# Optimization experiments

Measured on AMD Instinct MI355X. Metric: run time of the kernel, lower is better.

## Reference

```python
import jax, jax.numpy as jnp
import numpy as np

B, T, D = 64, 48, 16          # batch, time_depth, input_dim (n variables)
H = 128                       # n_units (== N_units, forced by decomp: y=h_mix has width n_units)
NU = 128                      # N_units
HEADS = 8
HEAD_DIM = H // HEADS
THR = 0.01                    # attention_threshold
LAM = 0.01                    # ridge_lambda
SHORT = 2

# All off-diagonal variable pairs. The torch code gathers only pairs in the batch-union of
# (a_t > 0) & ~eye; using ALL off-diagonal pairs is mathematically identical because excluded
# pairs have a_t == 0 for every batch element, giving all-zero phi columns whose ridge
# coefficients are exactly 0 and which do not perturb the other coefficients or h_hat.
_I, _J = np.nonzero(~np.eye(D, dtype=bool))
I_IDX = jnp.asarray(_I)
J_IDX = jnp.asarray(_J)
P = D * (D - 1)
K = 2 * D + P


def setup_inputs() -> dict:
    key = jax.random.key(0)
    ks = jax.random.split(key, 32)
    f32 = jnp.float32
    n = lambda k, shp, s: (jax.random.normal(k, shp, f32) * s)
    inp = {
        'x': jax.random.normal(ks[0], (B, T, D), f32),
        # per-variable LSTM params
        'W_j': n(ks[1], (D, H, H), 1.0 / np.sqrt(H)),
        'W_i': n(ks[2], (D, H, H), 1.0 / np.sqrt(H)),
        'W_f': n(ks[3], (D, H, H), 1.0 / np.sqrt(H)),
        'W_o': n(ks[4], (D, H, H), 1.0 / np.sqrt(H)),
        'U_j': n(ks[5], (D, 1, H), 0.3),
        'U_i': n(ks[6], (D, 1, H), 0.3),
        'U_f': n(ks[7], (D, 1, H), 0.3),
        'U_o': n(ks[8], (D, 1, H), 0.3),
        'B_j': jnp.full((D, H), 0.01, f32),
        'B_i': jnp.full((D, H), 0.01, f32),
        'B_f': jnp.full((D, H), 0.01, f32),
        'B_o': jnp.full((D, H), 0.01, f32),
        # mix LSTM params
        'u_j': n(ks[9], (D, NU), 0.3),
        'u_i': n(ks[10], (D, NU), 0.3),
        'u_f': n(ks[11], (D, NU), 0.3),
        'u_o': n(ks[12], (D, NU), 0.3),
        'w_j': n(ks[13], (NU, NU), 1.0 / np.sqrt(NU)),
        'w_i': n(ks[14], (NU, NU), 1.0 / np.sqrt(NU)),
        'w_f': n(ks[15], (NU, NU), 1.0 / np.sqrt(NU)),
        'w_o': n(ks[16], (NU, NU), 1.0 / np.sqrt(NU)),
        'b_j': jnp.full((NU,), 0.01, f32),
        'b_i': jnp.full((NU,), 0.01, f32),
        'b_f': jnp.full((NU,), 0.01, f32),
        'b_o': jnp.full((NU,), 0.01, f32),
        # attention params (torch Linear convention: y = x @ W.T)
        'W_qkv': n(ks[17], (3 * H, H), 1.0 / np.sqrt(H)),
        'W_out': n(ks[18], (H, H), 1.0 / np.sqrt(H)),
        # interaction decomposition psi projection
        'W_psi': n(ks[19], (H, H), 1.0 / np.sqrt(H)),
        'b_psi': jnp.full((H,), 0.01, f32),
        # prediction head
        'w_p': n(ks[20], (H, 1), 1.0 / np.sqrt(H)),
        'b_p': jnp.full((1,), 0.01, f32),
    }
    return inp


def _forward(x, W_j, W_i, W_f, W_o, U_j, U_i, U_f, U_o, B_j, B_i, B_f, B_o,
             u_j, u_i, u_f, u_o, w_j, w_i, w_f, w_o, b_j, b_i, b_f, b_o,
             W_qkv, W_out, W_psi, b_psi, w_p, b_p):
    f32 = x.dtype
    eyeK = LAM * jnp.eye(K, dtype=f32)

    def var_gate(h_var, x_t, W, U, Bp):
        # torch einsum('bij,ijk->bik') + einsum('bij,jik->bjk') with x_t unsqueezed
        return jnp.einsum('bdh,dhk->bdk', h_var, W) + x_t[:, :, None] * U[:, 0, :] + Bp

    def step(carry, inp):
        h_var, c_var, h_mix, c_mix = carry
        x_t, t = inp  # x_t: [B, D]
        h_prev = h_var
        # per-variable tensorized LSTM
        j_var = jnp.tanh(var_gate(h_var, x_t, W_j, U_j, B_j))
        i_var = jax.nn.sigmoid(var_gate(h_var, x_t, W_i, U_i, B_i))
        f_var = jax.nn.sigmoid(var_gate(h_var, x_t, W_f, U_f, B_f))
        o_var = jax.nn.sigmoid(var_gate(h_var, x_t, W_o, U_o, B_o))
        c_var = c_var * f_var + i_var * j_var
        h_var = o_var * jnp.tanh(c_var)
        delta_h = h_var - h_prev
        # mix LSTM
        i_t = jax.nn.sigmoid(x_t @ u_i + h_mix @ w_i + b_i)
        f_t = jax.nn.sigmoid(x_t @ u_f + h_mix @ w_f + b_f)
        o_t = jax.nn.sigmoid(x_t @ u_o + h_mix @ w_o + b_o)
        j_t = jnp.tanh(x_t @ u_j + h_mix @ w_j + b_j)
        c_mix = f_t * c_mix + i_t * j_t
        h_mix_lstm = o_t * jnp.tanh(c_mix)
        # multi-head cross-variable attention over the D variables
        qkv = h_var @ W_qkv.T                                  # [B, D, 3H]
        q, k, v = jnp.split(qkv, 3, axis=-1)
        q = q.reshape(B, D, HEADS, HEAD_DIM).transpose(0, 2, 1, 3)
        k = k.reshape(B, D, HEADS, HEAD_DIM).transpose(0, 2, 1, 3)
        v = v.reshape(B, D, HEADS, HEAD_DIM).transpose(0, 2, 1, 3)
        scores = jnp.einsum('bhqe,bhke->bhqk', q, k) / np.sqrt(HEAD_DIM).astype(np.float32)
        attn = jax.nn.softmax(scores, axis=-1)
        attn = jnp.where(attn >= THR, attn, jnp.zeros_like(attn))  # hard threshold, no renorm
        ctx = jnp.einsum('bhqk,bhke->bhqe', attn, v)
        ctx = ctx.transpose(0, 2, 1, 3).reshape(B, D, H)
        z = ctx @ W_out.T                                      # [B, D, H]
        a_t = attn.mean(axis=1)                                # [B, D, D]
        phi_long = jnp.swapaxes(h_prev, 1, 2)                  # [B, H, D]
        phi_short = jnp.swapaxes(delta_h, 1, 2)                # [B, H, D]
        pair = z[:, I_IDX, :] * z[:, J_IDX, :]                 # [B, P, H]
        psi = jnp.tanh(pair @ W_psi.T + b_psi)                 # [B, P, H]
        w = a_t[:, I_IDX, J_IDX][..., None]                    # [B, P, 1]
        phi_inter = jnp.swapaxes(psi * w, 1, 2)                # [B, H, P]
        phi = jnp.concatenate([phi_long, phi_short, phi_inter], axis=2)  # [B, H, K]
        A = jnp.einsum('bhk,bhl->bkl', phi, phi) + eyeK        # [B, K, K]
        bvec = jnp.einsum('bhk,bh->bk', phi, h_mix_lstm)       # [B, K]
        theta = jnp.linalg.solve(A, bvec[..., None])[..., 0]   # [B, K]
        h_hat = jnp.einsum('bhk,bk->bh', phi, theta)           # [B, H]
        alpha = theta[:, :D]
        beta = theta[:, D:2 * D]
        gamma = jnp.zeros((B, D, D), f32).at[:, I_IDX, J_IDX].set(theta[:, 2 * D:])
        pred_y = h_hat @ w_p + b_p                             # [B, 1]
        h_mix_new = jnp.where(t > SHORT, h_hat, h_mix_lstm)
        return (h_var, c_var, h_mix_new, c_mix), (pred_y, alpha, beta, gamma)

    h_var0 = jnp.zeros((B, D, H), f32)
    c_var0 = jnp.zeros((B, D, H), f32)
    h_mix0 = jnp.zeros((B, NU), f32)
    c_mix0 = jnp.zeros((B, NU), f32)
    ts = jnp.arange(T - 1)
    xs = (jnp.swapaxes(x, 0, 1)[:T - 1], ts)
    _, (preds, alphas, betas, gammas) = jax.lax.scan(step, (h_var0, c_var0, h_mix0, c_mix0), xs)
    s = SHORT + 1
    pred = jnp.swapaxes(preds[s:], 0, 1)   # [B, T-SHORT-2, 1]
    return pred, alphas[s:], betas[s:], gammas[s:]


def reference(x, W_j, W_i, W_f, W_o, U_j, U_i, U_f, U_o, B_j, B_i, B_f, B_o,
              u_j, u_i, u_f, u_o, w_j, w_i, w_f, w_o, b_j, b_i, b_f, b_o,
              W_qkv, W_out, W_psi, b_psi, w_p, b_p):
    return _forward(x, W_j, W_i, W_f, W_o, U_j, U_i, U_f, U_o, B_j, B_i, B_f, B_o,
                    u_j, u_i, u_f, u_o, w_j, w_i, w_f, w_o, b_j, b_i, b_f, b_o,
                    W_qkv, W_out, W_psi, b_psi, w_p, b_p)
```

## Files before the change

### kernel.cpp

```cpp
#include <hip/hip_runtime.h>
#include <hip/hip_bf16.h>
#include <math.h>

#define B_ 64
#define T_ 48
#define D_ 16
#define H_ 128
#define NU_ 128
#define LAM_ 0.01f
#define THR_ 0.01f

#define NSTEP_OUT 44
#define OFF_A (B_*NSTEP_OUT)
#define OFF_B (OFF_A + NSTEP_OUT*B_*D_)
#define OFF_G (OFF_B + NSTEP_OUT*B_*D_)

#define PHI_ROWS 240
#define PHI_STR  (PHI_ROWS*H_)
#define PHIBUF   (B_*PHI_STR)
#define GW_STR   12288
#define GBUF     (B_*GW_STR)
#define L_STR    16896
#define LBUF     (B_*L_STR)
#define PLS_STR  4096
#define PLSBUF   (B_*PLS_STR)

#define QKS 388
#define SCS 264

__device__ __forceinline__ float sigm(float v) { return 1.0f / (1.0f + expf(-v)); }
__device__ __forceinline__ float dot4(float4 a, float4 b) {
    return a.x*b.x + a.y*b.y + a.z*b.z + a.w*b.w;
}
__device__ __forceinline__ float rdlane(float v, int l) {
    return __uint_as_float(__builtin_amdgcn_readlane(__float_as_uint(v), l));
}


__global__ __launch_bounds__(256) void k_P(
    float* __restrict__ hv, float* __restrict__ cv,
    const float* __restrict__ gates, float* __restrict__ pls,
    const float* __restrict__ Wqkv, const float* __restrict__ Wout,
    float* __restrict__ z, float* __restrict__ at_g,
    const float* __restrict__ phi, float* __restrict__ Gring,
    const float* __restrict__ Lring,
    const float* __restrict__ hml, float* __restrict__ h_mix,
    const float* __restrict__ w_p, const float* __restrict__ b_p,
    float* __restrict__ out, int t)
{
    __shared__ __align__(16) float smem[12416];
    const int tid = threadIdx.x;
    const int bx = blockIdx.x;

    if (bx < 64) {
        const int ta = t + 2;
        if (ta < 0 || ta > T_ - 2) return;
        const int b = bx;
        const int BDH = B_*D_*H_;
        float* hs = smem;
        float* qk = smem + 2048;
        float* sc = smem + 8256;
        float* cx = smem + 10368;

        float* plsb = pls + ((size_t)(ta&3))*PLSBUF + (size_t)b*PLS_STR;
        const float4* g0 = (const float4*)(gates + b*2048);
        const float4* g1 = (const float4*)(gates + BDH + b*2048);
        const float4* g2 = (const float4*)(gates + 2*BDH + b*2048);
        const float4* g3 = (const float4*)(gates + 3*BDH + b*2048);
        float4* cv4 = (float4*)(cv + b*2048);
        float4* hv4 = (float4*)(hv + b*2048);
        float4* pl0 = (float4*)plsb;
        float4* pl1 = (float4*)(plsb + 16*H_);
        #pragma unroll
        for (int i = 0; i < 2; ++i) {
            int e4 = i*256 + tid;
            float4 jv = g0[e4], iv = g1[e4], fv = g2[e4], ov = g3[e4];
            float4 c = cv4[e4], ho = hv4[e4];
            float4 cn, hn, dl;
            cn.x = c.x*fv.x + iv.x*jv.x; hn.x = ov.x*tanhf(cn.x); dl.x = hn.x - ho.x;
            cn.y = c.y*fv.y + iv.y*jv.y; hn.y = ov.y*tanhf(cn.y); dl.y = hn.y - ho.y;
            cn.z = c.z*fv.z + iv.z*jv.z; hn.z = ov.z*tanhf(cn.z); dl.z = hn.z - ho.z;
            cn.w = c.w*fv.w + iv.w*jv.w; hn.w = ov.w*tanhf(cn.w); dl.w = hn.w - ho.w;
            cv4[e4] = cn; hv4[e4] = hn;
            ((float4*)hs)[e4] = hn;
            pl0[e4] = ho;
            pl1[e4] = dl;
        }
        __syncthreads();

        {
            const int half = tid >> 7, mt = tid & 127;
            const float4* w0 = (const float4*)(Wqkv + (size_t)(mt*3 + 0)*H_);
            const float4* w1 = (const float4*)(Wqkv + (size_t)(mt*3 + 1)*H_);
            const float4* w2 = (const float4*)(Wqkv + (size_t)(mt*3 + 2)*H_);
            float acc[3][8] = {};
            for (int i4 = 0; i4 < 32; i4++) {
                float4 wa = w0[i4], wb = w1[i4], wc = w2[i4];
                #pragma unroll
                for (int rr = 0; rr < 8; rr++) {
                    float4 h4 = *(const float4*)&hs[(half*8 + rr)*128 + i4*4];
                    acc[0][rr] += dot4(wa, h4);
                    acc[1][rr] += dot4(wb, h4);
                    acc[2][rr] += dot4(wc, h4);
                }
            }
            #pragma unroll
            for (int q = 0; q < 3; q++)
                #pragma unroll
                for (int rr = 0; rr < 8; rr++)
                    qk[(half*8 + rr)*QKS + mt*3 + q] = acc[q][rr];
        }
        __syncthreads();

        for (int e = tid; e < 2048; e += 256) {
            int hh2 = e >> 8, qd = (e >> 4) & 15, kd = e & 15;
            float s = 0.f;
            #pragma unroll
            for (int e4 = 0; e4 < 4; e4++)
                s += dot4(*(const float4*)&qk[qd*QKS + hh2*16 + e4*4],
                          *(const float4*)&qk[kd*QKS + 128 + hh2*16 + e4*4]);
            sc[hh2*SCS + qd*16 + kd] = s * 0.25f;
        }
        __syncthreads();

        if (tid < 128) {
            int hh2 = tid >> 4, qd = tid & 15;
            float mx = -1e30f;
            #pragma unroll
            for (int kd = 0; kd < 16; kd++) mx = fmaxf(mx, sc[hh2*SCS + qd*16 + kd]);
            float ex[16]; float s = 0.f;
            #pragma unroll
            for (int kd = 0; kd < 16; kd++) { ex[kd] = expf(sc[hh2*SCS + qd*16 + kd] - mx); s += ex[kd]; }
            float inv = 1.0f / s;
            #pragma unroll
            for (int kd = 0; kd < 16; kd++) {
                float a = ex[kd]*inv;
                sc[hh2*SCS + qd*16 + kd] = (a >= THR_) ? a : 0.0f;
            }
        }
        __syncthreads();

        {
            int qd = tid >> 4, kd = tid & 15;
            float s = 0.f;
            #pragma unroll
            for (int hh2 = 0; hh2 < 8; hh2++) s += sc[hh2*SCS + qd*16 + kd];
            at_g[b*256 + qd*16 + kd] = s * 0.125f;
        }

        for (int e = tid; e < 2048; e += 256) {
            int qd = e >> 7, c = e & 127, hh2 = c >> 4, ee = c & 15;
            float s = 0.f;
            #pragma unroll
            for (int kd = 0; kd < 16; kd++) s += sc[hh2*SCS + qd*16 + kd] * qk[kd*QKS + 256 + hh2*16 + ee];
            cx[qd*128 + c] = s;
        }
        __syncthreads();

        {
            int h = tid & 127, half = tid >> 7;
            const float4* wr = (const float4*)(Wout + (size_t)h*H_);
            float acc[8] = {};
            for (int i4 = 0; i4 < 32; i4++) {
                float4 w4 = wr[i4];
                #pragma unroll
                for (int r = 0; r < 8; r++)
                    acc[r] += dot4(w4, *(const float4*)&cx[(half*8 + r)*128 + i4*4]);
            }
            #pragma unroll
            for (int r = 0; r < 8; r++) z[b*2048 + (half*8 + r)*H_ + h] = acc[r];
        }
    } else if (bx < 256) {
        const int tg = t + 1;
        if (tg < 3 || tg > T_ - 2) return;
        const int tile = (bx - 64) >> 6, b = (bx - 64) & 63;
        const int r0 = (tile >= 1) ? 64 : 0;
        const int c0 = (tile == 2) ? 64 : 0;
        const bool diag = (r0 == c0);
        float* prt = smem;
        float* pct = smem + 1024;
        const float* pb   = phi + ((size_t)(tg%3))*PHIBUF + (size_t)b*PHI_STR;
        const float* plsb = pls + ((size_t)(tg&3))*PLSBUF + (size_t)b*PLS_STR;
        const int tr = tid >> 4, tc = tid & 15;
        const int kk = tid >> 4, rr4 = (tid & 15) << 2;
        float acc[4][4] = {};
        float4 vr, vc;

        {
            const float* src = (kk < 32) ? (plsb + (size_t)kk*H_) : (pb + (size_t)(kk - 32)*H_);
            vr = *(const float4*)&src[r0 + rr4];
            if (!diag) vc = *(const float4*)&src[c0 + rr4];
        }
        for (int kt = 0; kt < 17; kt++) {
            *(float4*)&prt[kk*64 + rr4] = vr;
            if (!diag) *(float4*)&pct[kk*64 + rr4] = vc;
            __syncthreads();
            if (kt < 16) {
                int krow = (kt + 1)*16 + kk;
                const float* src = (krow < 32) ? (plsb + (size_t)krow*H_)
                                               : (pb + (size_t)(krow - 32)*H_);
                vr = *(const float4*)&src[r0 + rr4];
                if (!diag) vc = *(const float4*)&src[c0 + rr4];
            }
            const float* pcb = diag ? prt : pct;
            #pragma unroll
            for (int k2 = 0; k2 < 16; k2++) {
                float4 a4 = *(const float4*)&prt[k2*64 + tr*4];
                float4 b4 = *(const float4*)&pcb[k2*64 + tc*4];
                float av[4] = {a4.x, a4.y, a4.z, a4.w};
                float bv[4] = {b4.x, b4.y, b4.z, b4.w};
                #pragma unroll
                for (int i = 0; i < 4; i++)
                    #pragma unroll
                    for (int j = 0; j < 4; j++)
                        acc[i][j] += av[i]*bv[j];
            }
            __syncthreads();
        }
        float* Gt = Gring + ((size_t)(tg&1))*GBUF + (size_t)b*GW_STR + (size_t)tile*4096;
        #pragma unroll
        for (int i = 0; i < 4; i++) {
            int lr = tr*4 + i;
            float v[4];
            #pragma unroll
            for (int j = 0; j < 4; j++) {
                int lc = tc*4 + j;
                v[j] = acc[i][j] + ((diag && lr == lc) ? LAM_ : 0.0f);
            }
            float4 o; o.x = v[0]; o.y = v[1]; o.z = v[2]; o.w = v[3];
            *(float4*)&Gt[lr*64 + tc*4] = o;
        }
    } else {
        const int tv = t - 1;
        if (tv < 0 || tv > T_ - 2) return;
        const int b = bx - 256;
        if (tv < 3) {
            if (tid < 128) h_mix[b*128 + tid] = hml[b*128 + tid];
            return;
        }
        float* ys = smem;
        const float* Lb = Lring + ((size_t)(tv&1))*LBUF + (size_t)b*L_STR;

        if (tid < 64) {
            __builtin_amdgcn_s_setprio(1);
            const int lane = tid;
            float hm0 = hml[b*128 + lane];
            float hm1 = hml[b*128 + lane + 64];
            float dv0 = Lb[lane*132 + 128];
            float dv1 = Lb[(lane+64)*132 + 128];
            float acc0 = hm0, acc1 = hm1;

            {
                float c0[16], c1[16], n0[16], n1[16];
                #pragma unroll
                for (int k = 0; k < 16; ++k) {
                    c0[k] = Lb[k*132 + lane];
                    c1[k] = Lb[k*132 + lane + 64];
                }
                for (int g = 0; g < 4; ++g) {
                    if (g < 3) {
                        #pragma unroll
                        for (int k = 0; k < 16; ++k) {
                            n0[k] = Lb[(16*(g+1)+k)*132 + lane];
                            n1[k] = Lb[(16*(g+1)+k)*132 + lane + 64];
                        }
                    }
                    const int s = 16*g;
                    #pragma unroll
                    for (int k = 0; k < 16; ++k) {
                        int j = s + k;
                        float yj = rdlane(acc0 * dv0, j);
                        if (lane > j) acc0 -= c0[k]*yj;
                        else if (lane == j) acc0 = yj;
                        acc1 -= c1[k]*yj;
                    }
                    #pragma unroll
                    for (int k = 0; k < 16; ++k) { c0[k] = n0[k]; c1[k] = n1[k]; }
                }
            }
            {
                float c1[16], n1[16];
                #pragma unroll
                for (int k = 0; k < 16; ++k) c1[k] = Lb[(64+k)*132 + lane + 64];
                for (int g = 0; g < 4; ++g) {
                    if (g < 3) {
                        #pragma unroll
                        for (int k = 0; k < 16; ++k)
                            n1[k] = Lb[(64+16*(g+1)+k)*132 + lane + 64];
                    }
                    #pragma unroll
                    for (int k = 0; k < 16; ++k) {
                        int j = 16*g + k;
                        float yj = rdlane(acc1 * dv1, j);
                        if (lane > j) acc1 -= c1[k]*yj;
                        else if (lane == j) acc1 = yj;
                    }
                    #pragma unroll
                    for (int k = 0; k < 16; ++k) c1[k] = n1[k];
                }
            }
            ys[lane] = acc0;
            ys[lane + 64] = acc1;

            for (int p = 7; p >= 0; --p) {
                const int s = p*16;
                float br = 0.f, minv = 0.f;
                float lc[16];
                if (lane < 16) {
                    br = ys[s + lane];
                    minv = Lb[(s+lane)*132 + 128];
                    #pragma unroll
                    for (int k4 = 0; k4 < 4; ++k4) {
                        float4 f4 = *(const float4*)&Lb[(s+lane)*132 + s + k4*4];
                        lc[k4*4+0]=f4.x; lc[k4*4+1]=f4.y; lc[k4*4+2]=f4.z; lc[k4*4+3]=f4.w;
                    }
                } else {
                    #pragma unroll
                    for (int k = 0; k < 16; ++k) lc[k] = 0.f;
                }
                float xk[16];
                #pragma unroll
                for (int j = 15; j >= 0; --j) {
                    if (lane == j) br *= minv;
                    float xj = rdlane(br, j);
                    if (lane < j) br -= lc[j]*xj;
                    xk[j] = xj;
                }
                if (lane < 16) ys[s + lane] = br;
                for (int i = lane; i < s; i += 64) {
                    float a = ys[i];
                    #pragma unroll
                    for (int k4 = 0; k4 < 4; ++k4) {
                        float4 f4 = *(const float4*)&Lb[i*132 + s + k4*4];
                        a -= f4.x*xk[k4*4] + f4.y*xk[k4*4+1] + f4.z*xk[k4*4+2] + f4.w*xk[k4*4+3];
                    }
                    ys[i] = a;
                }
            }

            float y0 = ys[lane], y1 = ys[lane + 64];
            float hh0 = hm0 - LAM_*y0, hh1 = hm1 - LAM_*y1;
            h_mix[b*128 + lane]      = hh0;
            h_mix[b*128 + lane + 64] = hh1;
            float pw = hh0 * w_p[lane] + hh1 * w_p[lane + 64];
            for (int off = 32; off; off >>= 1) pw += __shfl_down(pw, off);
            if (lane == 0) out[b*NSTEP_OUT + (tv - 3)] = pw + b_p[0];
            __builtin_amdgcn_s_setprio(0);
        }
        __syncthreads();

        {
            const int ts = tv - 3;
            const float* plsb = pls + ((size_t)(tv&3))*PLSBUF + (size_t)b*PLS_STR;
            const float* phb  = phi + ((size_t)(tv%3))*PHIBUF + (size_t)b*PHI_STR;
            const float4* y4  = (const float4*)ys;
            for (int k = tid; k < 272; k += 256) {
                const float* rowp = (k < 32) ? plsb + (size_t)k*H_
                                             : phb + (size_t)(k - 32)*H_;
                const float4* r4 = (const float4*)rowp;
                float th = 0.f;
                #pragma unroll
                for (int i4 = 0; i4 < 32; i4++) th += dot4(r4[i4], y4[i4]);
                if (k < 16)
                    out[OFF_A + ts*(B_*D_) + b*D_ + k] = th;
                else if (k < 32)
                    out[OFF_B + ts*(B_*D_) + b*D_ + (k - 16)] = th;
                else {
                    int p = k - 32, ip = p/15, jj = p%15, jp = jj + (jj >= ip ? 1 : 0);
                    out[OFF_G + ts*(B_*D_*D_) + b*(D_*D_) + ip*D_ + jp] = th;
                }
            }
            if (tid < D_)
                out[OFF_G + ts*(B_*D_*D_) + b*(D_*D_) + tid*D_ + tid] = 0.0f;
        }
    }
}

__global__ __launch_bounds__(256) void k_Q(
    const float* __restrict__ z, const float* __restrict__ at,
    const float* __restrict__ Wpsi, const float* __restrict__ bpsi,
    float* __restrict__ phi,
    const float* __restrict__ x, const float* __restrict__ hv,
    const float* __restrict__ Wj, const float* __restrict__ Wi, const float* __restrict__ Wf, const float* __restrict__ Wo,
    const float* __restrict__ Uj, const float* __restrict__ Ui, const float* __restrict__ Uf, const float* __restrict__ Uo,
    const float* __restrict__ Bj, const float* __restrict__ Bi, const float* __restrict__ Bf, const float* __restrict__ Bo,
    float* __restrict__ gates,
    const float* __restrict__ Gring, float* __restrict__ Lring,
    const float* __restrict__ h_mix, float* __restrict__ c_mix, float* __restrict__ hml,
    const float* __restrict__ uj, const float* __restrict__ ui, const float* __restrict__ uf, const float* __restrict__ uo,
    const float* __restrict__ wj, const float* __restrict__ wi, const float* __restrict__ wf, const float* __restrict__ wo,
    const float* __restrict__ bj, const float* __restrict__ bi, const float* __restrict__ bf_, const float* __restrict__ bo,
    int t)
{
    __shared__ __align__(16) float smem[8448];
    const int tid = threadIdx.x;
    const int bx = blockIdx.x;

    if (bx < 128) {
        const int tf = t + (bx >> 6);
        if ((t & 1) || tf < 3 || tf > T_ - 2) return;
        const int b = bx & 63;
        float* Pan = smem;

        const int R = tid >> 4, C = tid & 15;
        const bool lower = (C <= R);

        float g[8][8] = {};
        if (lower) {
            const int tsel = (C >= 8) ? 2 : ((R >= 8) ? 1 : 0);
            const float* Gt = Gring + ((size_t)(tf&1))*GBUF + (size_t)b*GW_STR + (size_t)tsel*4096;
            const int lcb = C*8 - ((C >= 8) ? 64 : 0);
            #pragma unroll
            for (int r = 0; r < 8; ++r) {
                const int lr = R*8 + r - ((R >= 8) ? 64 : 0);
                float4 lo = *(const float4*)(Gt + lr*64 + lcb);
                float4 hi = *(const float4*)(Gt + lr*64 + lcb + 4);
                g[r][0]=lo.x; g[r][1]=lo.y; g[r][2]=lo.z; g[r][3]=lo.w;
                g[r][4]=hi.x; g[r][5]=hi.y; g[r][6]=hi.z; g[r][7]=hi.w;
            }
        }

        float* Lb = Lring + ((size_t)(tf&1))*LBUF + (size_t)b*L_STR;

        for (int p = 0; p < 8; ++p) {
            const int s = p*16;
            if ((C >> 1) == p && R >= 2*p) {
                #pragma unroll
                for (int c = 0; c < 8; ++c) {
                    const int lc = ((C & 1) << 3) + c;
                    float4 lo = {g[0][c], g[1][c], g[2][c], g[3][c]};
                    float4 hi = {g[4][c], g[5][c], g[6][c], g[7][c]};
                    *(float4*)&Pan[lc*132 + R*8]     = lo;
                    *(float4*)&Pan[lc*132 + R*8 + 4] = hi;
                }
            }
            __syncthreads();
            if (tid < 64) {
                const int lane = tid;
                const int r0 = s + lane, r1 = r0 + 64;
                const bool v0 = r0 < 128, v1 = r1 < 128;
                float a0[16], a1[16];
                #pragma unroll
                for (int k = 0; k < 16; ++k) {
                    a0[k] = v0 ? Pan[k*132 + r0] : 0.f;
                    a1[k] = v1 ? Pan[k*132 + r1] : 0.f;
                }
                float myinv = 0.f;
                #pragma unroll
                for (int j = 0; j < 16; ++j) {
                    float piv = rdlane(a0[j], j);
                    float inv = rsqrtf(piv);
                    float dsq = piv * inv;
                    if (lane == j) myinv = inv;
                    a0[j] = (lane == j) ? dsq : a0[j]*inv;
                    a1[j] *= inv;
                    #pragma unroll
                    for (int c = j+1; c < 16; ++c) {
                        float Lcj = rdlane(a0[j], c);
                        a0[c] -= a0[j]*Lcj;
                        a1[c] -= a1[j]*Lcj;
                    }
                }
                if (lane < 16) Lb[(s+lane)*132 + 128] = myinv;
                #pragma unroll
                for (int k = 0; k < 16; ++k) {
                    if (v0) { Pan[k*132 + r0] = a0[k]; Lb[(s+k)*132 + r0] = a0[k]; }
                    if (v1) { Pan[k*132 + r1] = a1[k]; Lb[(s+k)*132 + r1] = a1[k]; }
                }
            }
            __syncthreads();
            if (lower && C >= 2*(p+1)) {
                const float* colp = Pan;
                float4 r04 = *(const float4*)&colp[R*8];
                float4 r14 = *(const float4*)&colp[R*8 + 4];
                float4 c04 = *(const float4*)&colp[C*8];
                float4 c14 = *(const float4*)&colp[C*8 + 4];
                #pragma unroll
                for (int k = 0; k < 16; ++k) {
                    float lr[8] = {r04.x,r04.y,r04.z,r04.w,r14.x,r14.y,r14.z,r14.w};
                    float lc[8] = {c04.x,c04.y,c04.z,c04.w,c14.x,c14.y,c14.z,c14.w};
                    if (k < 15) {
                        const float* coln = &Pan[(k+1)*132];
                        r04 = *(const float4*)&coln[R*8];
                        r14 = *(const float4*)&coln[R*8 + 4];
                        c04 = *(const float4*)&coln[C*8];
                        c14 = *(const float4*)&coln[C*8 + 4];
                    }
                    #pragma unroll
                    for (int r = 0; r < 8; ++r)
                        #pragma unroll
                        for (int c = 0; c < 8; ++c)
                            g[r][c] -= lr[r]*lc[c];
                }
            }
            __syncthreads();
        }
    } else if (bx < 448) {
        const int tp = t + 2;
        if (tp < 3 || tp > T_ - 2) return;
        const int pc = (bx - 128) >> 6, b = (bx - 128) & 63;
        const int p0 = pc * 48;
        float* zs = smem;
        float* pr = smem + 2048;

        {
            const float4* zsrc = (const float4*)(z + b*2048);
            #pragma unroll
            for (int i = 0; i < 2; ++i) ((float4*)zs)[i*256 + tid] = zsrc[i*256 + tid];
        }
        __syncthreads();
        for (int e = tid; e < 48*128; e += 256) {
            int pp = e >> 7, c = e & 127;
            int p = p0 + pp, ip = p/15, jj2 = p%15, jp = jj2 + (jj2 >= ip ? 1 : 0);
            pr[pp*128 + c] = zs[ip*128 + c] * zs[jp*128 + c];
        }
        __syncthreads();

        const int hg = tid & 31, pg = tid >> 5;
        const int h0 = hg*4, pp0 = pg*6;
        const float4* w0 = (const float4*)(Wpsi + (size_t)(h0+0)*H_);
        const float4* w1 = (const float4*)(Wpsi + (size_t)(h0+1)*H_);
        const float4* w2 = (const float4*)(Wpsi + (size_t)(h0+2)*H_);
        const float4* w3 = (const float4*)(Wpsi + (size_t)(h0+3)*H_);
        float acc[6][4] = {};
        for (int i4 = 0; i4 < 32; i4++) {
            float4 wa = w0[i4], wb = w1[i4], wc = w2[i4], wd = w3[i4];
            #pragma unroll
            for (int r = 0; r < 6; r++) {
                float4 p4 = *(const float4*)&pr[(pp0 + r)*128 + i4*4];
                acc[r][0] += dot4(wa, p4);
                acc[r][1] += dot4(wb, p4);
                acc[r][2] += dot4(wc, p4);
                acc[r][3] += dot4(wd, p4);
            }
        }
        float4 bb = *(const float4*)&bpsi[h0];
        float* phb = phi + ((size_t)(tp%3))*PHIBUF + (size_t)b*PHI_STR;
        #pragma unroll
        for (int r = 0; r < 6; r++) {
            int pp = pp0 + r, p = p0 + pp;
            int ip = p/15, jj2 = p%15, jp = jj2 + (jj2 >= ip ? 1 : 0);
            float wat = at[b*256 + ip*16 + jp];
            float4 o;
            o.x = tanhf(acc[r][0] + bb.x) * wat;
            o.y = tanhf(acc[r][1] + bb.y) * wat;
            o.z = tanhf(acc[r][2] + bb.z) * wat;
            o.w = tanhf(acc[r][3] + bb.w) * wat;
            *(float4*)&phb[(size_t)p*H_ + h0] = o;
        }
    } else if (bx < 576) {
        const int tn = t + 3;
        if (tn < 0 || tn > T_ - 2) return;
        float* hsT = smem;
        float* Ws  = smem + 4352;
        const int fbx = bx - 448;
        const int kh = fbx & 1, g = (fbx >> 1) & 3, d = fbx >> 3;
        const int k0 = kh * 64;
        const float* W  = (g==0?Wj:(g==1?Wi:(g==2?Wf:Wo))) + (size_t)d*H_*H_;
        const float* U  = (g==0?Uj:(g==1?Ui:(g==2?Uf:Uo))) + d*H_;
        const float* Bp = (g==0?Bj:(g==1?Bi:(g==2?Bf:Bo))) + d*H_;

        const int tb = tid >> 4, tk = tid & 15;
        float acc[4][4] = {};

        for (int hc = 0; hc < 2; hc++) {
            __syncthreads();
            for (int e = tid; e < 64*64; e += 256) {
                int b2 = e >> 6, h2 = e & 63;
                hsT[h2*68 + b2] = hv[(b2*D_ + d)*H_ + hc*64 + h2];
            }
            for (int e = tid; e < 64*64; e += 256) {
                int h2 = e >> 6, kk = e & 63;
                Ws[h2*64 + kk] = W[(hc*64 + h2)*H_ + k0 + kk];
            }
            __syncthreads();
            for (int h2 = 0; h2 < 64; h2++) {
                float4 hb = *(const float4*)&hsT[h2*68 + tb*4];
                float4 wk = *(const float4*)&Ws[h2*64 + tk*4];
                float hbv[4] = {hb.x, hb.y, hb.z, hb.w};
                float wkv[4] = {wk.x, wk.y, wk.z, wk.w};
                #pragma unroll
                for (int a2 = 0; a2 < 4; a2++)
                    #pragma unroll
                    for (int c2 = 0; c2 < 4; c2++)
                        acc[a2][c2] += hbv[a2] * wkv[c2];
            }
        }

        float u4[4], bp4[4];
        #pragma unroll
        for (int c2 = 0; c2 < 4; c2++) { u4[c2] = U[k0 + tk*4 + c2]; bp4[c2] = Bp[k0 + tk*4 + c2]; }

        #pragma unroll
        for (int a2 = 0; a2 < 4; a2++) {
            int b2 = tb*4 + a2;
            float xv = x[(b2*T_ + tn)*D_ + d];
            float4 o;
            float pre[4];
            #pragma unroll
            for (int c2 = 0; c2 < 4; c2++) pre[c2] = acc[a2][c2] + xv*u4[c2] + bp4[c2];
            if (g == 0) { o.x = tanhf(pre[0]); o.y = tanhf(pre[1]); o.z = tanhf(pre[2]); o.w = tanhf(pre[3]); }
            else        { o.x = sigm(pre[0]);  o.y = sigm(pre[1]);  o.z = sigm(pre[2]);  o.w = sigm(pre[3]); }
            *(float4*)&gates[(size_t)g*(B_*D_*H_) + (b2*D_ + d)*H_ + k0 + tk*4] = o;
        }
    } else {
        const int tm = t;
        if (tm < 0 || tm > T_ - 2) return;
        const int b = bx - 576;
        float* xs  = smem;
        float* hs2 = smem + 16;
        float* gj  = smem + 144;
        float* gi  = smem + 272;
        float* gf  = smem + 400;
        float* go  = smem + 528;
        const int n = tid & 127, gg = tid >> 7;
        if (tid < 16)  xs[tid]  = x[(b*T_ + tm)*D_ + tid];
        if (tid < 128) hs2[tid] = h_mix[b*NU_ + tid];
        __syncthreads();

        const float* uA = gg ? uf : uj;
        const float* uB = gg ? uo : ui;
        const float* wA = gg ? wf : wj;
        const float* wB = gg ? wo : wi;
        float accA = gg ? bf_[n] : bj[n];
        float accB = gg ? bo[n]  : bi[n];
        #pragma unroll
        for (int d2 = 0; d2 < 16; ++d2) {
            float xv = xs[d2];
            accA += xv * uA[d2*NU_ + n];
            accB += xv * uB[d2*NU_ + n];
        }
        for (int m = 0; m < 128; ++m) {
            float hvv = hs2[m];
            accA += hvv * wA[m*NU_ + n];
            accB += hvv * wB[m*NU_ + n];
        }
        if (gg == 0) { gj[n] = tanhf(accA); gi[n] = sigm(accB); }
        else         { gf[n] = sigm(accA);  go[n] = sigm(accB); }
        __syncthreads();
        if (tid < 128) {
            float cn = gf[tid]*c_mix[b*NU_ + tid] + gi[tid]*gj[tid];
            c_mix[b*NU_ + tid] = cn;
            hml[b*NU_ + tid]   = go[tid]*tanhf(cn);
        }
    }
}


__global__ __launch_bounds__(256) void k_X8(
    float* __restrict__ hv, float* __restrict__ cv,
    const float* __restrict__ gates, float* __restrict__ pls,
    const float* __restrict__ Wqkv, const float* __restrict__ Wout,
    float* __restrict__ z, float* __restrict__ at_g,
    const float* __restrict__ phi, float* __restrict__ Gw,
    const float* __restrict__ x, const float* __restrict__ h_mix,
    float* __restrict__ c_mix, float* __restrict__ hml,
    const float* __restrict__ uj, const float* __restrict__ ui, const float* __restrict__ uf, const float* __restrict__ uo,
    const float* __restrict__ wj, const float* __restrict__ wi, const float* __restrict__ wf, const float* __restrict__ wo,
    const float* __restrict__ bj, const float* __restrict__ bi, const float* __restrict__ bf_, const float* __restrict__ bo,
    const float* __restrict__ ybuf, float* __restrict__ out,
    int ta, int tg, int tm, int te)
{
    __shared__ __align__(16) float smem[12416];
    const int tid = threadIdx.x;
    const int bx = blockIdx.x;

    if (bx < 64) {
        if (ta < 0) return;
        const int b = bx;
        const int BDH = B_*D_*H_;
        float* hs = smem;
        float* qk = smem + 2048;
        float* sc = smem + 8256;
        float* cx = smem + 10368;

        float* plsb = pls + ((size_t)(ta&3)*B_ + b)*PLS_STR;
        const float4* g0 = (const float4*)(gates + b*2048);
        const float4* g1 = (const float4*)(gates + BDH + b*2048);
        const float4* g2 = (const float4*)(gates + 2*BDH + b*2048);
        const float4* g3 = (const float4*)(gates + 3*BDH + b*2048);
        float4* cv4 = (float4*)(cv + b*2048);
        float4* hv4 = (float4*)(hv + b*2048);
        float4* pl0 = (float4*)plsb;
        float4* pl1 = (float4*)(plsb + 16*H_);
        #pragma unroll
        for (int i = 0; i < 2; ++i) {
            int e4 = i*256 + tid;
            float4 jv = g0[e4], iv = g1[e4], fv = g2[e4], ov = g3[e4];
            float4 c = cv4[e4], ho = hv4[e4];
            float4 cn, hn, dl;
            cn.x = c.x*fv.x + iv.x*jv.x; hn.x = ov.x*tanhf(cn.x); dl.x = hn.x - ho.x;
            cn.y = c.y*fv.y + iv.y*jv.y; hn.y = ov.y*tanhf(cn.y); dl.y = hn.y - ho.y;
            cn.z = c.z*fv.z + iv.z*jv.z; hn.z = ov.z*tanhf(cn.z); dl.z = hn.z - ho.z;
            cn.w = c.w*fv.w + iv.w*jv.w; hn.w = ov.w*tanhf(cn.w); dl.w = hn.w - ho.w;
            cv4[e4] = cn; hv4[e4] = hn;
            ((float4*)hs)[e4] = hn;
            pl0[e4] = ho;
            pl1[e4] = dl;
        }
        __syncthreads();
        {
            const int half = tid >> 7, mt = tid & 127;
            const float4* w0 = (const float4*)(Wqkv + (size_t)(mt*3 + 0)*H_);
            const float4* w1 = (const float4*)(Wqkv + (size_t)(mt*3 + 1)*H_);
            const float4* w2 = (const float4*)(Wqkv + (size_t)(mt*3 + 2)*H_);
            float acc[3][8] = {};
            for (int i4 = 0; i4 < 32; i4++) {
                float4 wa = w0[i4], wb = w1[i4], wc = w2[i4];
                #pragma unroll
                for (int rr = 0; rr < 8; rr++) {
                    float4 h4 = *(const float4*)&hs[(half*8 + rr)*128 + i4*4];
                    acc[0][rr] += dot4(wa, h4);
                    acc[1][rr] += dot4(wb, h4);
                    acc[2][rr] += dot4(wc, h4);
                }
            }
            #pragma unroll
            for (int q = 0; q < 3; q++)
                #pragma unroll
                for (int rr = 0; rr < 8; rr++)
                    qk[(half*8 + rr)*QKS + mt*3 + q] = acc[q][rr];
        }
        __syncthreads();
        for (int e = tid; e < 2048; e += 256) {
            int hh2 = e >> 8, qd = (e >> 4) & 15, kd = e & 15;
            float s = 0.f;
            #pragma unroll
            for (int e4 = 0; e4 < 4; e4++)
                s += dot4(*(const float4*)&qk[qd*QKS + hh2*16 + e4*4],
                          *(const float4*)&qk[kd*QKS + 128 + hh2*16 + e4*4]);
            sc[hh2*SCS + qd*16 + kd] = s * 0.25f;
        }
        __syncthreads();
        if (tid < 128) {
            int hh2 = tid >> 4, qd = tid & 15;
            float mx = -1e30f;
            #pragma unroll
            for (int kd = 0; kd < 16; kd++) mx = fmaxf(mx, sc[hh2*SCS + qd*16 + kd]);
            float ex[16]; float s = 0.f;
            #pragma unroll
            for (int kd = 0; kd < 16; kd++) { ex[kd] = expf(sc[hh2*SCS + qd*16 + kd] - mx); s += ex[kd]; }
            float inv = 1.0f / s;
            #pragma unroll
            for (int kd = 0; kd < 16; kd++) {
                float a = ex[kd]*inv;
                sc[hh2*SCS + qd*16 + kd] = (a >= THR_) ? a : 0.0f;
            }
        }
        __syncthreads();
        {
            int qd = tid >> 4, kd = tid & 15;
            float s = 0.f;
            #pragma unroll
            for (int hh2 = 0; hh2 < 8; hh2++) s += sc[hh2*SCS + qd*16 + kd];
            at_g[b*256 + qd*16 + kd] = s * 0.125f;
        }
        for (int e = tid; e < 2048; e += 256) {
            int qd = e >> 7, c = e & 127, hh2 = c >> 4, ee = c & 15;
            float s = 0.f;
            #pragma unroll
            for (int kd = 0; kd < 16; kd++) s += sc[hh2*SCS + qd*16 + kd] * qk[kd*QKS + 256 + hh2*16 + ee];
// ... 330 lines not shown
            const float4* zsrc = (const float4*)(z + b*2048);
            #pragma unroll
            for (int i = 0; i < 2; ++i) ((float4*)zs)[i*256 + tid] = zsrc[i*256 + tid];
        }
        __syncthreads();
        for (int e = tid; e < 48*128; e += 256) {
            int pp = e >> 7, c = e & 127;
            int p = p0 + pp, ip = p/15, jj2 = p%15, jp = jj2 + (jj2 >= ip ? 1 : 0);
            pr[pp*128 + c] = zs[ip*128 + c] * zs[jp*128 + c];
        }
        __syncthreads();
        const int hg = tid & 31, pg = tid >> 5;
        const int h0 = hg*4, pp0 = pg*6;
        const float4* w0 = (const float4*)(Wpsi + (size_t)(h0+0)*H_);
        const float4* w1 = (const float4*)(Wpsi + (size_t)(h0+1)*H_);
        const float4* w2 = (const float4*)(Wpsi + (size_t)(h0+2)*H_);
        const float4* w3 = (const float4*)(Wpsi + (size_t)(h0+3)*H_);
        float acc[6][4] = {};
        for (int i4 = 0; i4 < 32; i4++) {
            float4 wa = w0[i4], wb = w1[i4], wc = w2[i4], wd = w3[i4];
            #pragma unroll
            for (int r = 0; r < 6; r++) {
                float4 p4 = *(const float4*)&pr[(pp0 + r)*128 + i4*4];
                acc[r][0] += dot4(wa, p4);
                acc[r][1] += dot4(wb, p4);
                acc[r][2] += dot4(wc, p4);
                acc[r][3] += dot4(wd, p4);
            }
        }
        float4 bb = *(const float4*)&bpsi[h0];
        float* phb = phi + (size_t)(tp&1)*PHIBUF + (size_t)b*PHI_STR;
        #pragma unroll
        for (int r = 0; r < 6; r++) {
            int pp = pp0 + r, p = p0 + pp;
            int ip = p/15, jj2 = p%15, jp = jj2 + (jj2 >= ip ? 1 : 0);
            float wat = at[b*256 + ip*16 + jp];
            float4 o;
            o.x = tanhf(acc[r][0] + bb.x) * wat;
            o.y = tanhf(acc[r][1] + bb.y) * wat;
            o.z = tanhf(acc[r][2] + bb.z) * wat;
            o.w = tanhf(acc[r][3] + bb.w) * wat;
            *(float4*)&phb[(size_t)p*H_ + h0] = o;
        }
    } else {
        if (tf < 0 || tf > T_ - 2) return;
        float* hsT = smem;
        float* Ws  = smem + 8704;
        const int fbx = bx - 384;
        const int kh = fbx & 1, g = (fbx >> 1) & 3, d = fbx >> 3;
        const int k0 = kh * 64;
        const float* W  = (g==0?Wj:(g==1?Wi:(g==2?Wf:Wo))) + (size_t)d*H_*H_;
        const float* U  = (g==0?Uj:(g==1?Ui:(g==2?Uf:Uo))) + d*H_;
        const float* Bp = (g==0?Bj:(g==1?Bi:(g==2?Bf:Bo))) + d*H_;

        for (int e = tid; e < 64*128; e += 256) {
            int b2 = e >> 7, h2 = e & 127;
            hsT[h2*68 + b2] = hv[(b2*D_ + d)*H_ + h2];
        }
        const int tb = tid >> 4, tk = tid & 15;
        float acc[4][4] = {};
        for (int hc = 0; hc < 2; hc++) {
            __syncthreads();
            for (int e = tid; e < 64*64; e += 256) {
                int h2 = e >> 6, kk = e & 63;
                Ws[h2*64 + kk] = W[(hc*64 + h2)*H_ + k0 + kk];
            }
            __syncthreads();
            for (int h2 = 0; h2 < 64; h2++) {
                float4 hb = *(const float4*)&hsT[(hc*64 + h2)*68 + tb*4];
                float4 wk = *(const float4*)&Ws[h2*64 + tk*4];
                float hbv[4] = {hb.x, hb.y, hb.z, hb.w};
                float wkv[4] = {wk.x, wk.y, wk.z, wk.w};
                #pragma unroll
                for (int a2 = 0; a2 < 4; a2++)
                    #pragma unroll
                    for (int c2 = 0; c2 < 4; c2++)
                        acc[a2][c2] += hbv[a2] * wkv[c2];
            }
        }
        float u4[4], bp4[4];
        #pragma unroll
        for (int c2 = 0; c2 < 4; c2++) { u4[c2] = U[k0 + tk*4 + c2]; bp4[c2] = Bp[k0 + tk*4 + c2]; }
        #pragma unroll
        for (int a2 = 0; a2 < 4; a2++) {
            int b2 = tb*4 + a2;
            float xv = x[(b2*T_ + tf)*D_ + d];
            float4 o;
            float pre[4];
            #pragma unroll
            for (int c2 = 0; c2 < 4; c2++) pre[c2] = acc[a2][c2] + xv*u4[c2] + bp4[c2];
            if (g == 0) { o.x = tanhf(pre[0]); o.y = tanhf(pre[1]); o.z = tanhf(pre[2]); o.w = tanhf(pre[3]); }
            else        { o.x = sigm(pre[0]);  o.y = sigm(pre[1]);  o.z = sigm(pre[2]);  o.w = sigm(pre[3]); }
            *(float4*)&gates[(size_t)g*(B_*D_*H_) + (b2*D_ + d)*H_ + k0 + tk*4] = o;
        }
    }
}

extern "C" void kernel_launch(void* const* d_in, const int* in_sizes, int n_in,
                              void* d_out, int out_size, void* d_ws, size_t ws_size,
                              hipStream_t stream) {
    const float* x    = (const float*)d_in[0];
    const float* W_j  = (const float*)d_in[1];
    const float* W_i  = (const float*)d_in[2];
    const float* W_f  = (const float*)d_in[3];
    const float* W_o  = (const float*)d_in[4];
    const float* U_j  = (const float*)d_in[5];
    const float* U_i  = (const float*)d_in[6];
    const float* U_f  = (const float*)d_in[7];
    const float* U_o  = (const float*)d_in[8];
    const float* B_j  = (const float*)d_in[9];
    const float* B_i  = (const float*)d_in[10];
    const float* B_f  = (const float*)d_in[11];
    const float* B_o  = (const float*)d_in[12];
    const float* u_j  = (const float*)d_in[13];
    const float* u_i  = (const float*)d_in[14];
    const float* u_f  = (const float*)d_in[15];
    const float* u_o  = (const float*)d_in[16];
    const float* w_j  = (const float*)d_in[17];
    const float* w_i  = (const float*)d_in[18];
    const float* w_f  = (const float*)d_in[19];
    const float* w_o  = (const float*)d_in[20];
    const float* b_j  = (const float*)d_in[21];
    const float* b_i  = (const float*)d_in[22];
    const float* b_f  = (const float*)d_in[23];
    const float* b_o  = (const float*)d_in[24];
    const float* W_qkv= (const float*)d_in[25];
    const float* W_out= (const float*)d_in[26];
    const float* W_psi= (const float*)d_in[27];
    const float* b_psi= (const float*)d_in[28];
    const float* w_p  = (const float*)d_in[29];
    const float* b_p  = (const float*)d_in[30];

    float* out = (float*)d_out;
    float* ws = (float*)d_ws;

    const size_t NEED = (size_t)11640832 * 4;

    if (ws_size >= NEED) {
        float* hv    = ws;
        float* cv    = hv + 131072;
        float* h_mix = cv + 131072;
        float* c_mix = h_mix + 8192;
        float* hml   = c_mix + 8192;
        float* gates = hml + 8192;
        float* zbuf  = gates + 524288;
        float* atbuf = zbuf + 131072;
        float* pls   = atbuf + 16384;
        float* phi   = pls + 4*262144;
        float* Gring = phi + (size_t)3*1966080;
        float* Lring = Gring + 2*786432;

        hipMemsetAsync(ws, 0, (size_t)286720 * sizeof(float), stream);

        #define LAUNCH_P(tt) k_P<<<320, 256, 0, stream>>>( \
            hv, cv, gates, pls, W_qkv, W_out, zbuf, atbuf, phi, Gring, Lring, \
            hml, h_mix, w_p, b_p, out, (tt))
        #define LAUNCH_Q(tt) k_Q<<<640, 256, 0, stream>>>( \
            zbuf, atbuf, W_psi, b_psi, phi, x, hv, \
            W_j, W_i, W_f, W_o, U_j, U_i, U_f, U_o, B_j, B_i, B_f, B_o, gates, \
            Gring, Lring, h_mix, c_mix, hml, \
            u_j, u_i, u_f, u_o, w_j, w_i, w_f, w_o, b_j, b_i, b_f, b_o, (tt))

        LAUNCH_Q(-3);
        LAUNCH_P(-2);
        LAUNCH_Q(-2);
        LAUNCH_P(-1);
        LAUNCH_Q(-1);

        for (int t = 0; t <= 47; ++t) {
            LAUNCH_P(t);
            if (t < 47) LAUNCH_Q(t);
        }
        #undef LAUNCH_P
        #undef LAUNCH_Q
    } else {
        float* h_var = ws;
        float* c_var = h_var + 131072;
        float* h_mix = c_var + 131072;
        float* c_mix = h_mix + 8192;
        float* hml   = c_mix + 8192;
        float* gates = hml + 8192;
        float* phi   = gates + 524288;
        float* zbuf  = phi + 3932160;
        float* atbuf = zbuf + 131072;
        float* Gw    = atbuf + 16384;
        float* pls   = Gw + 786432;
        float* ybuf  = pls + 1048576;

        hipMemsetAsync(ws, 0, (size_t)278528 * sizeof(float), stream);

        k_Y8<<<512, 256, 0, stream>>>(
            zbuf, atbuf, W_psi, b_psi, phi, x, h_var,
            W_j, W_i, W_f, W_o, U_j, U_i, U_f, U_o, B_j, B_i, B_f, B_o, gates,
            Gw, hml, h_mix, w_p, b_p, ybuf, out, -1, 0, -1);

        for (int t = 0; t < T_ - 1; t++) {
            k_X8<<<448, 256, 0, stream>>>(
                h_var, c_var, gates, pls, W_qkv, W_out, zbuf, atbuf,
                phi, Gw, x, h_mix, c_mix, hml,
                u_j, u_i, u_f, u_o, w_j, w_i, w_f, w_o, b_j, b_i, b_f, b_o,
                ybuf, out, t, t - 1, t - 1, t - 2);
            k_Y8<<<512, 256, 0, stream>>>(
                zbuf, atbuf, W_psi, b_psi, phi, x, h_var,
                W_j, W_i, W_f, W_o, U_j, U_i, U_f, U_o, B_j, B_i, B_f, B_o, gates,
                Gw, hml, h_mix, w_p, b_p, ybuf, out, t, t + 1, t - 1);
        }
        k_X8<<<448, 256, 0, stream>>>(
            h_var, c_var, gates, pls, W_qkv, W_out, zbuf, atbuf,
            phi, Gw, x, h_mix, c_mix, hml,
            u_j, u_i, u_f, u_o, w_j, w_i, w_f, w_o, b_j, b_i, b_f, b_o,
            ybuf, out, -1, T_ - 2, T_ - 2, T_ - 3);
        k_Y8<<<512, 256, 0, stream>>>(
            zbuf, atbuf, W_psi, b_psi, phi, x, h_var,
            W_j, W_i, W_f, W_o, U_j, U_i, U_f, U_o, B_j, B_i, B_f, B_o, gates,
            Gw, hml, h_mix, w_p, b_p, ybuf, out, -1, -1, T_ - 2);
        k_X8<<<448, 256, 0, stream>>>(
            h_var, c_var, gates, pls, W_qkv, W_out, zbuf, atbuf,
            phi, Gw, x, h_mix, c_mix, hml,
            u_j, u_i, u_f, u_o, w_j, w_i, w_f, w_o, b_j, b_i, b_f, b_o,
            ybuf, out, -1, -1, -1, T_ - 2);
    }
}
```

Baseline: 3.367 ms.

## Move blocked Cholesky factorization from k_Q into k_P, one timestep per launch

The per-batch blocked Cholesky of the ridge Gram matrix moves out of k_Q, where it ran on alternate steps for two timesteps at once, into extra blocks of k_P that factor one timestep per launch. The shared-memory panel is double-buffered, which drops the trailing barrier per panel. Each factored panel is copied to the global L buffer with a coalesced float4 copy instead of scattered per-lane stores. The aim is to even out per-step critical-path work and cut barrier and store overhead, at the cost of a longer-running k_P and a dependence on G being ready one launch earlier.

```diff
diff --git a/kernel.cpp b/kernel.cpp
--- a/kernel.cpp
+++ b/kernel.cpp
@@ -43,7 +43,7 @@
     const float* __restrict__ Wqkv, const float* __restrict__ Wout,
     float* __restrict__ z, float* __restrict__ at_g,
     const float* __restrict__ phi, float* __restrict__ Gring,
-    const float* __restrict__ Lring,
+    float* __restrict__ Lring,
     const float* __restrict__ hml, float* __restrict__ h_mix,
     const float* __restrict__ w_p, const float* __restrict__ b_p,
     float* __restrict__ out, int t)
@@ -230,7 +230,7 @@
             float4 o; o.x = v[0]; o.y = v[1]; o.z = v[2]; o.w = v[3];
             *(float4*)&Gt[lr*64 + tc*4] = o;
         }
-    } else {
+    } else if (bx < 320) {
         const int tv = t - 1;
         if (tv < 0 || tv > T_ - 2) return;
         const int b = bx - 256;
@@ -373,6 +373,110 @@
             if (tid < D_)
                 out[OFF_G + ts*(B_*D_*D_) + b*(D_*D_) + tid*D_ + tid] = 0.0f;
         }
+    } else {
+        const int tf = t;
+        if (tf < 3 || tf > T_ - 2) return;
+        const int b = bx - 320;
+        float* Pan = smem;
+
+        const int R = tid >> 4, C = tid & 15;
+        const bool lower = (C <= R);
+
+        float g[8][8] = {};
+        if (lower) {
+            const int tsel = (C >= 8) ? 2 : ((R >= 8) ? 1 : 0);
+            const float* Gt = Gring + ((size_t)(tf&1))*GBUF + (size_t)b*GW_STR + (size_t)tsel*4096;
+            const int lcb = C*8 - ((C >= 8) ? 64 : 0);
+            #pragma unroll
+            for (int r = 0; r < 8; ++r) {
+                const int lr = R*8 + r - ((R >= 8) ? 64 : 0);
+                float4 lo = *(const float4*)(Gt + lr*64 + lcb);
+                float4 hi = *(const float4*)(Gt + lr*64 + lcb + 4);
+                g[r][0]=lo.x; g[r][1]=lo.y; g[r][2]=lo.z; g[r][3]=lo.w;
+                g[r][4]=hi.x; g[r][5]=hi.y; g[r][6]=hi.z; g[r][7]=hi.w;
+            }
+        }
+
+        float* Lb = Lring + ((size_t)(tf&1))*LBUF + (size_t)b*L_STR;
+
+        for (int p = 0; p < 8; ++p) {
+            const int s = p*16;
+            float* Pc = Pan + (p & 1)*2112;
+            if ((C >> 1) == p && R >= 2*p) {
+                #pragma unroll
+                for (int c = 0; c < 8; ++c) {
+                    const int lc = ((C & 1) << 3) + c;
+                    float4 lo = {g[0][c], g[1][c], g[2][c], g[3][c]};
+                    float4 hi = {g[4][c], g[5][c], g[6][c], g[7][c]};
+                    *(float4*)&Pc[lc*132 + R*8]     = lo;
+                    *(float4*)&Pc[lc*132 + R*8 + 4] = hi;
+                }
+            }
+            __syncthreads();
+            if (tid < 64) {
+                const int lane = tid;
+                const int r0 = s + lane, r1 = r0 + 64;
+                const bool v0 = r0 < 128, v1 = r1 < 128;
+                float a0[16], a1[16];
+                #pragma unroll
+                for (int k = 0; k < 16; ++k) {
+                    a0[k] = v0 ? Pc[k*132 + r0] : 0.f;
+                    a1[k] = v1 ? Pc[k*132 + r1] : 0.f;
+                }
+                float myinv = 0.f;
+                #pragma unroll
+                for (int j = 0; j < 16; ++j) {
+                    float piv = rdlane(a0[j], j);
+                    float inv = rsqrtf(piv);
+                    float dsq = piv * inv;
+                    if (lane == j) myinv = inv;
+                    a0[j] = (lane == j) ? dsq : a0[j]*inv;
+                    a1[j] *= inv;
+                    #pragma unroll
+                    for (int c = j+1; c < 16; ++c) {
+                        float Lcj = rdlane(a0[j], c);
+                        a0[c] -= a0[j]*Lcj;
+                        a1[c] -= a1[j]*Lcj;
+                    }
+                }
+                if (lane < 16) Pc[lane*132 + 128] = myinv;
+                #pragma unroll
+                for (int k = 0; k < 16; ++k) {
+                    if (v0) Pc[k*132 + r0] = a0[k];
+                    if (v1) Pc[k*132 + r1] = a1[k];
+                }
+            }
+            __syncthreads();
+            {
+                const float4* s4 = (const float4*)Pc;
+                float4* d4 = (float4*)(Lb + (size_t)s*132);
+                for (int e = tid; e < 528; e += 256) d4[e] = s4[e];
+            }
+            if (lower && C >= 2*(p+1)) {
+                const float* colp = Pc;
+                float4 r04 = *(const float4*)&colp[R*8];
+                float4 r14 = *(const float4*)&colp[R*8 + 4];
+                float4 c04 = *(const float4*)&colp[C*8];
+                float4 c14 = *(const float4*)&colp[C*8 + 4];
+                #pragma unroll
+                for (int k = 0; k < 16; ++k) {
+                    float lr[8] = {r04.x,r04.y,r04.z,r04.w,r14.x,r14.y,r14.z,r14.w};
+                    float lc[8] = {c04.x,c04.y,c04.z,c04.w,c14.x,c14.y,c14.z,c14.w};
+                    if (k < 15) {
+                        const float* coln = &Pc[(k+1)*132];
+                        r04 = *(const float4*)&coln[R*8];
+                        r14 = *(const float4*)&coln[R*8 + 4];
+                        c04 = *(const float4*)&coln[C*8];
+                        c14 = *(const float4*)&coln[C*8 + 4];
+                    }
+                    #pragma unroll
+                    for (int r = 0; r < 8; ++r)
+                        #pragma unroll
+                        for (int c = 0; c < 8; ++c)
+                            g[r][c] -= lr[r]*lc[c];
+                }
+            }
+        }
     }
 }
 
@@ -385,7 +489,6 @@
     const float* __restrict__ Uj, const float* __restrict__ Ui, const float* __restrict__ Uf, const float* __restrict__ Uo,
     const float* __restrict__ Bj, const float* __restrict__ Bi, const float* __restrict__ Bf, const float* __restrict__ Bo,
     float* __restrict__ gates,
-    const float* __restrict__ Gring, float* __restrict__ Lring,
     const float* __restrict__ h_mix, float* __restrict__ c_mix, float* __restrict__ hml,
     const float* __restrict__ uj, const float* __restrict__ ui, const float* __restrict__ uf, const float* __restrict__ uo,
     const float* __restrict__ wj, const float* __restrict__ wi, const float* __restrict__ wf, const float* __restrict__ wo,
@@ -396,109 +499,10 @@
     const int tid = threadIdx.x;
     const int bx = blockIdx.x;
 
-    if (bx < 128) {
-        const int tf = t + (bx >> 6);
-        if ((t & 1) || tf < 3 || tf > T_ - 2) return;
-        const int b = bx & 63;
-        float* Pan = smem;
-
-        const int R = tid >> 4, C = tid & 15;
-        const bool lower = (C <= R);
-
-        float g[8][8] = {};
-        if (lower) {
-            const int tsel = (C >= 8) ? 2 : ((R >= 8) ? 1 : 0);
-            const float* Gt = Gring + ((size_t)(tf&1))*GBUF + (size_t)b*GW_STR + (size_t)tsel*4096;
-            const int lcb = C*8 - ((C >= 8) ? 64 : 0);
-            #pragma unroll
-            for (int r = 0; r < 8; ++r) {
-                const int lr = R*8 + r - ((R >= 8) ? 64 : 0);
-                float4 lo = *(const float4*)(Gt + lr*64 + lcb);
-                float4 hi = *(const float4*)(Gt + lr*64 + lcb + 4);
-                g[r][0]=lo.x; g[r][1]=lo.y; g[r][2]=lo.z; g[r][3]=lo.w;
-                g[r][4]=hi.x; g[r][5]=hi.y; g[r][6]=hi.z; g[r][7]=hi.w;
-            }
-        }
-
-        float* Lb = Lring + ((size_t)(tf&1))*LBUF + (size_t)b*L_STR;
-
-        for (int p = 0; p < 8; ++p) {
-            const int s = p*16;
-            if ((C >> 1) == p && R >= 2*p) {
-                #pragma unroll
-                for (int c = 0; c < 8; ++c) {
-                    const int lc = ((C & 1) << 3) + c;
-                    float4 lo = {g[0][c], g[1][c], g[2][c], g[3][c]};
-                    float4 hi = {g[4][c], g[5][c], g[6][c], g[7][c]};
-                    *(float4*)&Pan[lc*132 + R*8]     = lo;
-                    *(float4*)&Pan[lc*132 + R*8 + 4] = hi;
-                }
-            }
-            __syncthreads();
-            if (tid < 64) {
-                const int lane = tid;
-                const int r0 = s + lane, r1 = r0 + 64;
-                const bool v0 = r0 < 128, v1 = r1 < 128;
-                float a0[16], a1[16];
-                #pragma unroll
-                for (int k = 0; k < 16; ++k) {
-                    a0[k] = v0 ? Pan[k*132 + r0] : 0.f;
-                    a1[k] = v1 ? Pan[k*132 + r1] : 0.f;
-                }
-                float myinv = 0.f;
-                #pragma unroll
-                for (int j = 0; j < 16; ++j) {
-                    float piv = rdlane(a0[j], j);
-                    float inv = rsqrtf(piv);
-                    float dsq = piv * inv;
-                    if (lane == j) myinv = inv;
-                    a0[j] = (lane == j) ? dsq : a0[j]*inv;
-                    a1[j] *= inv;
-                    #pragma unroll
-                    for (int c = j+1; c < 16; ++c) {
-                        float Lcj = rdlane(a0[j], c);
-                        a0[c] -= a0[j]*Lcj;
-                        a1[c] -= a1[j]*Lcj;
-                    }
-                }
-                if (lane < 16) Lb[(s+lane)*132 + 128] = myinv;
-                #pragma unroll
-                for (int k = 0; k < 16; ++k) {
-                    if (v0) { Pan[k*132 + r0] = a0[k]; Lb[(s+k)*132 + r0] = a0[k]; }
-                    if (v1) { Pan[k*132 + r1] = a1[k]; Lb[(s+k)*132 + r1] = a1[k]; }
-                }
-            }
-            __syncthreads();
-            if (lower && C >= 2*(p+1)) {
-                const float* colp = Pan;
-                float4 r04 = *(const float4*)&colp[R*8];
-                float4 r14 = *(const float4*)&colp[R*8 + 4];
-                float4 c04 = *(const float4*)&colp[C*8];
-                float4 c14 = *(const float4*)&colp[C*8 + 4];
-                #pragma unroll
-                for (int k = 0; k < 16; ++k) {
-                    float lr[8] = {r04.x,r04.y,r04.z,r04.w,r14.x,r14.y,r14.z,r14.w};
-                    float lc[8] = {c04.x,c04.y,c04.z,c04.w,c14.x,c14.y,c14.z,c14.w};
-                    if (k < 15) {
-                        const float* coln = &Pan[(k+1)*132];
-                        r04 = *(const float4*)&coln[R*8];
-                        r14 = *(const float4*)&coln[R*8 + 4];
-                        c04 = *(const float4*)&coln[C*8];
-                        c14 = *(const float4*)&coln[C*8 + 4];
-                    }
-                    #pragma unroll
-                    for (int r = 0; r < 8; ++r)
-                        #pragma unroll
-                        for (int c = 0; c < 8; ++c)
-                            g[r][c] -= lr[r]*lc[c];
-                }
-            }
-            __syncthreads();
-        }
-    } else if (bx < 448) {
+    if (bx < 320) {
         const int tp = t + 2;
         if (tp < 3 || tp > T_ - 2) return;
-        const int pc = (bx - 128) >> 6, b = (bx - 128) & 63;
+        const int pc = bx >> 6, b = bx & 63;
         const int p0 = pc * 48;
         float* zs = smem;
         float* pr = smem + 2048;
@@ -548,12 +552,12 @@
             o.w = tanhf(acc[r][3] + bb.w) * wat;
             *(float4*)&phb[(size_t)p*H_ + h0] = o;
         }
-    } else if (bx < 576) {
+    } else if (bx < 448) {
         const int tn = t + 3;
         if (tn < 0 || tn > T_ - 2) return;
         float* hsT = smem;
         float* Ws  = smem + 4352;
-        const int fbx = bx - 448;
+        const int fbx = bx - 320;
         const int kh = fbx & 1, g = (fbx >> 1) & 3, d = fbx >> 3;
         const int k0 = kh * 64;
         const float* W  = (g==0?Wj:(g==1?Wi:(g==2?Wf:Wo))) + (size_t)d*H_*H_;
@@ -606,7 +610,7 @@
     } else {
         const int tm = t;
         if (tm < 0 || tm > T_ - 2) return;
-        const int b = bx - 576;
+        const int b = bx - 448;
         float* xs  = smem;
         float* hs2 = smem + 16;
         float* gj  = smem + 144;
@@ -1243,13 +1247,13 @@
 
         hipMemsetAsync(ws, 0, (size_t)286720 * sizeof(float), stream);
 
-        #define LAUNCH_P(tt) k_P<<<320, 256, 0, stream>>>( \
+        #define LAUNCH_P(tt) k_P<<<384, 256, 0, stream>>>( \
             hv, cv, gates, pls, W_qkv, W_out, zbuf, atbuf, phi, Gring, Lring, \
             hml, h_mix, w_p, b_p, out, (tt))
-        #define LAUNCH_Q(tt) k_Q<<<640, 256, 0, stream>>>( \
+        #define LAUNCH_Q(tt) k_Q<<<512, 256, 0, stream>>>( \
             zbuf, atbuf, W_psi, b_psi, phi, x, hv, \
             W_j, W_i, W_f, W_o, U_j, U_i, U_f, U_o, B_j, B_i, B_f, B_o, gates, \
-            Gring, Lring, h_mix, c_mix, hml, \
+            h_mix, c_mix, hml, \
             u_j, u_i, u_f, u_o, w_j, w_i, w_f, w_o, b_j, b_i, b_f, b_o, (tt))
 
         LAUNCH_Q(-3);
```

New measurement: 3.839 ms. +14.0%, slower.
